# Kernel optimization log

Measured on AMD Instinct MI355X. Metric: run time of the kernel, lower is better.

The kernel has to match this reference:

```python
import jax, jax.numpy as jnp
import numpy as np
from jax import lax

K = 25
SIGMA = 9.0
PAD = K // 2


def _gaussian_kernel():
    # 1D gaussian, normalized, then outer product -> depthwise (3,1,K,K) kernel
    coords = jnp.arange(K, dtype=jnp.float32) - (K // 2)
    g = jnp.exp(-coords ** 2 / (2.0 * SIGMA ** 2))
    g = g / g.sum()
    k2d = jnp.outer(g, g)  # (K, K)
    return jnp.broadcast_to(k2d[None, None], (3, 1, K, K))


def setup_inputs() -> dict:
    key = jax.random.key(0)
    x = jax.random.uniform(key, (32, 3, 512, 512), dtype=jnp.float32)
    return {"x": x}


def reference(x):
    kernel = _gaussian_kernel()
    y = lax.conv_general_dilated(
        x, kernel,
        window_strides=(1, 1),
        padding=[(PAD, PAD), (PAD, PAD)],
        dimension_numbers=("NCHW", "OIHW", "NCHW"),
        feature_group_count=3,
    )
    return jnp.clip(y, 0.0, 1.0)
```

## Files before the change

kernel.cpp:

```cpp
#include <hip/hip_runtime.h>

#define NB 32
#define CC 3
#define HH 512
#define WW 512
#define KS 25
#define PAD 12
#define HT 8
#define LDSW 536

__device__ __forceinline__ float clamp01(float v) {
    return fminf(fmaxf(v, 0.0f), 1.0f);
}

__global__ __launch_bounds__(256, 4) void gblur_fused(const float* __restrict__ x,
                                                      float* __restrict__ out) {
    constexpr float W[KS] = {
        0.02181520f, 0.02514307f, 0.02862302f, 0.03218484f, 0.03574584f,
        0.03921371f, 0.04249020f, 0.04547544f, 0.04807347f, 0.05019624f,
        0.05176967f, 0.05273727f, 0.05306384f, 0.05273727f, 0.05176967f,
        0.05019624f, 0.04807347f, 0.04547544f, 0.04249020f, 0.03921371f,
        0.03574584f, 0.03218484f, 0.02862302f, 0.02514307f, 0.02181520f};

    __shared__ float tile[HT * LDSW];

    int tid = threadIdx.x;

    if (tid < HT * 2 * PAD) {
        int r = tid / (2 * PAD);
        int k = tid - r * (2 * PAD);
        tile[r * LDSW + (k < PAD ? k : 512 + k)] = 0.0f;
    }

    int b = blockIdx.x;
    const int nwg = NB * CC * (HH / HT);
    int per = nwg >> 3;
    int swz = (b & 7) * per + (b >> 3);
    int plane = swz >> 6;
    int strip = swz & 63;
    int r0 = strip * HT;

    const float* ibase = x + (long)plane * (HH * WW);
    float*       obase = out + (long)plane * (HH * WW);

    int col4 = tid & 127;
    int rg = (tid >> 7) * 4;
    const float* ip = ibase + col4 * 4;

    float4 acc0 = make_float4(0.f, 0.f, 0.f, 0.f);
    float4 acc1 = acc0, acc2 = acc0, acc3 = acc0;

#pragma unroll
    for (int r = 0; r < 4 + KS - 1; ++r) {
        int rr = r0 + rg - PAD + r;
        float4 v = make_float4(0.f, 0.f, 0.f, 0.f);
        if (rr >= 0 && rr < HH)
            v = *(const float4*)(ip + (long)rr * WW);
        if (r - 0 >= 0 && r - 0 < KS) { float w = W[r];     acc0.x += v.x*w; acc0.y += v.y*w; acc0.z += v.z*w; acc0.w += v.w*w; }
        if (r - 1 >= 0 && r - 1 < KS) { float w = W[r - 1]; acc1.x += v.x*w; acc1.y += v.y*w; acc1.z += v.z*w; acc1.w += v.w*w; }
        if (r - 2 >= 0 && r - 2 < KS) { float w = W[r - 2]; acc2.x += v.x*w; acc2.y += v.y*w; acc2.z += v.z*w; acc2.w += v.w*w; }
        if (r - 3 >= 0 && r - 3 < KS) { float w = W[r - 3]; acc3.x += v.x*w; acc3.y += v.y*w; acc3.z += v.z*w; acc3.w += v.w*w; }
    }
    *(float4*)&tile[(rg + 0) * LDSW + PAD + col4 * 4] = acc0;
    *(float4*)&tile[(rg + 1) * LDSW + PAD + col4 * 4] = acc1;
    *(float4*)&tile[(rg + 2) * LDSW + PAD + col4 * 4] = acc2;
    *(float4*)&tile[(rg + 3) * LDSW + PAD + col4 * 4] = acc3;

    __syncthreads();

#pragma unroll
    for (int it = 0; it < 4; ++it) {
        int f = it * 256 + tid;
        int c4 = f & 127;
        int row = f >> 7;
        const float* lp = &tile[row * LDSW + c4 * 4];
        float o0 = 0.f, o1 = 0.f, o2 = 0.f, o3 = 0.f;
#pragma unroll
        for (int q = 0; q < 7; ++q) {
            float4 v = *(const float4*)(lp + 4 * q);
            float vv[4] = {v.x, v.y, v.z, v.w};
#pragma unroll
            for (int e = 0; e < 4; ++e) {
                int wdx = 4 * q + e;
                if (wdx - 0 >= 0 && wdx - 0 < KS) o0 += vv[e] * W[wdx];
                if (wdx - 1 >= 0 && wdx - 1 < KS) o1 += vv[e] * W[wdx - 1];
                if (wdx - 2 >= 0 && wdx - 2 < KS) o2 += vv[e] * W[wdx - 2];
                if (wdx - 3 >= 0 && wdx - 3 < KS) o3 += vv[e] * W[wdx - 3];
            }
        }
        float4 ov = make_float4(clamp01(o0), clamp01(o1), clamp01(o2), clamp01(o3));
        *(float4*)(obase + (long)(r0 + row) * WW + c4 * 4) = ov;
    }
}

extern "C" void kernel_launch(void* const* d_in, const int* in_sizes, int n_in,
                              void* d_out, int out_size, void* d_ws, size_t ws_size,
                              hipStream_t stream) {
    const float* x = (const float*)d_in[0];
    float* out = (float*)d_out;
    const int nwg = NB * CC * (HH / HT);
    gblur_fused<<<nwg, 256, 0, stream>>>(x, out);
}
```

Measured before the change: 48.30 us.

## Compute all 8 rows per thread on float2 columns and specialize interior strips

The vertical pass now has each thread own two columns and accumulate all eight output rows, instead of four columns over four rows. Each thread reads 32 input rows rather than 28, but the two thread halves no longer load overlapping halo rows, so total global loads per block drop. A template flag gives interior strips a version with no row bounds checks. The trade-off is narrower 8-byte loads instead of 16-byte loads, and 16 accumulator pairs that raise register pressure under the 4-wave launch bound.

```diff
diff --git a/kernel.cpp b/kernel.cpp
--- a/kernel.cpp
+++ b/kernel.cpp
@@ -13,8 +13,10 @@
     return fminf(fmaxf(v, 0.0f), 1.0f);
 }
 
-__global__ __launch_bounds__(256, 4) void gblur_fused(const float* __restrict__ x,
-                                                      float* __restrict__ out) {
+template<bool EDGE>
+__device__ __forceinline__ void blur_body(const float* __restrict__ ibase,
+                                          float* __restrict__ obase,
+                                          int r0, int tid, float* tile) {
     constexpr float W[KS] = {
         0.02181520f, 0.02514307f, 0.02862302f, 0.03218484f, 0.03574584f,
         0.03921371f, 0.04249020f, 0.04547544f, 0.04807347f, 0.05019624f,
@@ -22,49 +24,35 @@
         0.05019624f, 0.04807347f, 0.04547544f, 0.04249020f, 0.03921371f,
         0.03574584f, 0.03218484f, 0.02862302f, 0.02514307f, 0.02181520f};
 
-    __shared__ float tile[HT * LDSW];
-
-    int tid = threadIdx.x;
-
     if (tid < HT * 2 * PAD) {
         int r = tid / (2 * PAD);
         int k = tid - r * (2 * PAD);
         tile[r * LDSW + (k < PAD ? k : 512 + k)] = 0.0f;
     }
 
-    int b = blockIdx.x;
-    const int nwg = NB * CC * (HH / HT);
-    int per = nwg >> 3;
-    int swz = (b & 7) * per + (b >> 3);
-    int plane = swz >> 6;
-    int strip = swz & 63;
-    int r0 = strip * HT;
-
-    const float* ibase = x + (long)plane * (HH * WW);
-    float*       obase = out + (long)plane * (HH * WW);
-
-    int col4 = tid & 127;
-    int rg = (tid >> 7) * 4;
-    const float* ip = ibase + col4 * 4;
-
-    float4 acc0 = make_float4(0.f, 0.f, 0.f, 0.f);
-    float4 acc1 = acc0, acc2 = acc0, acc3 = acc0;
+    const float* ip = ibase + tid * 2;
+    float2 acc[HT];
+#pragma unroll
+    for (int j = 0; j < HT; ++j) acc[j] = make_float2(0.f, 0.f);
 
 #pragma unroll
-    for (int r = 0; r < 4 + KS - 1; ++r) {
-        int rr = r0 + rg - PAD + r;
-        float4 v = make_float4(0.f, 0.f, 0.f, 0.f);
-        if (rr >= 0 && rr < HH)
-            v = *(const float4*)(ip + (long)rr * WW);
-        if (r - 0 >= 0 && r - 0 < KS) { float w = W[r];     acc0.x += v.x*w; acc0.y += v.y*w; acc0.z += v.z*w; acc0.w += v.w*w; }
-        if (r - 1 >= 0 && r - 1 < KS) { float w = W[r - 1]; acc1.x += v.x*w; acc1.y += v.y*w; acc1.z += v.z*w; acc1.w += v.w*w; }
-        if (r - 2 >= 0 && r - 2 < KS) { float w = W[r - 2]; acc2.x += v.x*w; acc2.y += v.y*w; acc2.z += v.z*w; acc2.w += v.w*w; }
-        if (r - 3 >= 0 && r - 3 < KS) { float w = W[r - 3]; acc3.x += v.x*w; acc3.y += v.y*w; acc3.z += v.z*w; acc3.w += v.w*w; }
+    for (int r = 0; r < HT + KS - 1; ++r) {
+        int rr = r0 - PAD + r;
+        float2 v = make_float2(0.f, 0.f);
+        if (!EDGE || (rr >= 0 && rr < HH))
+            v = *(const float2*)(ip + (long)rr * WW);
+#pragma unroll
+        for (int j = 0; j < HT; ++j) {
+            int t = r - j;
+            if (t >= 0 && t < KS) {
+                acc[j].x += v.x * W[t];
+                acc[j].y += v.y * W[t];
+            }
+        }
     }
-    *(float4*)&tile[(rg + 0) * LDSW + PAD + col4 * 4] = acc0;
-    *(float4*)&tile[(rg + 1) * LDSW + PAD + col4 * 4] = acc1;
-    *(float4*)&tile[(rg + 2) * LDSW + PAD + col4 * 4] = acc2;
-    *(float4*)&tile[(rg + 3) * LDSW + PAD + col4 * 4] = acc3;
+#pragma unroll
+    for (int j = 0; j < HT; ++j)
+        *(float2*)&tile[j * LDSW + PAD + tid * 2] = acc[j];
 
     __syncthreads();
 
@@ -93,6 +81,29 @@
     }
 }
 
+__global__ __launch_bounds__(256, 4) void gblur_fused(const float* __restrict__ x,
+                                                      float* __restrict__ out) {
+    __shared__ float tile[HT * LDSW];
+
+    int tid = threadIdx.x;
+
+    int b = blockIdx.x;
+    const int nwg = NB * CC * (HH / HT);
+    int per = nwg >> 3;
+    int swz = (b & 7) * per + (b >> 3);
+    int plane = swz >> 6;
+    int strip = swz & 63;
+    int r0 = strip * HT;
+
+    const float* ibase = x + (long)plane * (HH * WW);
+    float*       obase = out + (long)plane * (HH * WW);
+
+    if (r0 >= PAD && r0 <= HH - HT - PAD)
+        blur_body<false>(ibase, obase, r0, tid, tile);
+    else
+        blur_body<true>(ibase, obase, r0, tid, tile);
+}
+
 extern "C" void kernel_launch(void* const* d_in, const int* in_sizes, int n_in,
                               void* d_out, int out_size, void* d_ws, size_t ws_size,
                               hipStream_t stream) {
```

Result: faster. 43.61 us (-9.7%).
